# Kernel optimization log

Measured on AMD Instinct MI355X. Metric: run time of the kernel, lower is better.

## Reference

```python
import jax, jax.numpy as jnp
import numpy as np

# Broyden low-rank inverse-Jacobian matvecs. Us: [b,d,e,T], VTs: [b,T,d,e], x: [b,d,e].
# Unwritten history slots are zero, so using the full buffers equals torch's :nstep slicing.

def _matvec(Us, VTs, x):
    VTx = jnp.einsum('btde,bde->bt', VTs, x)
    return -x + jnp.einsum('bdet,bt->bde', Us, VTx)

def _rmatvec(Us, VTs, x):
    xTU = jnp.einsum('bde,bdet->bt', x, Us)
    return -x + jnp.einsum('bt,btde->bde', xTU, VTs)

def broyden(g, x0, threshold, eps):
    """Faithful port of broyden(..., ls=False): line search returns s=1 always."""
    B, D, E = x0.shape
    T = min(threshold, 27)
    gx0 = g(x0)
    init_obj = jnp.linalg.norm(gx0)
    protect = init_obj * (1e6 * E)  # protect_thres = 1e6 * n_elem
    Us0 = jnp.zeros((B, D, E, T), x0.dtype)
    VTs0 = jnp.zeros((B, T, D, E), x0.dtype)

    def cond(s):
        nstep, x, gx, upd, Us, VTs, obj, low, lx, lg = s
        return (obj >= eps) & (nstep < threshold) & (obj <= protect)

    def body(s):
        nstep, x, gx, upd, Us, VTs, obj, low, lx, lg = s
        x_new = x + upd                     # step size s = 1 (ls off)
        gx_new = g(x_new)
        dx, dg = upd, gx_new - gx
        nstep = nstep + 1
        obj_new = jnp.linalg.norm(gx_new)
        better = obj_new < low
        low = jnp.where(better, obj_new, low)
        lx = jnp.where(better, x_new, lx)
        lg = jnp.where(better, gx_new, lg)
        # Broyden rank-1 update of the inverse-Jacobian history
        vT = _rmatvec(Us, VTs, dx)
        denom = jnp.einsum('bde,bde->b', vT, dg)
        u = (dx - _matvec(Us, VTs, dg)) / denom[:, None, None]
        vT = jnp.where(jnp.isnan(vT), 0.0, vT)
        u = jnp.where(jnp.isnan(u), 0.0, u)
        Us = Us.at[:, :, :, (nstep - 1) % T].set(u)
        VTs = VTs.at[:, (nstep - 1) % T].set(vT)
        upd = -_matvec(Us, VTs, gx_new)
        return (nstep, x_new, gx_new, upd, Us, VTs, obj_new, low, lx, lg)

    s0 = (jnp.int32(0), x0, gx0, gx0, Us0, VTs0, init_obj, init_obj, x0, gx0)
    s = jax.lax.while_loop(cond, body, s0)
    return s[8], jnp.linalg.norm(s[9])  # lowest_xest, ||lowest_gx||


def f_layer(z, x, W, U, b):
    return jnp.tanh(z @ W + x @ U + b)


def setup_inputs() -> dict:
    key = jax.random.key(0)
    k1, k2, k3, k4 = jax.random.split(key, 4)
    B, D = 256, 2048
    x = jax.random.normal(k1, (B, D), jnp.float32)
    initial_point = jnp.zeros((B, D), jnp.float32)
    W = jax.random.normal(k2, (D, D), jnp.float32) * (0.4 / np.sqrt(D))  # contractive in z
    U = jax.random.normal(k3, (D, D), jnp.float32) * (1.0 / np.sqrt(D))
    b = jax.random.normal(k4, (D,), jnp.float32) * 0.01
    return {"x": x, "initial_point": initial_point, "W": W, "U": U, "b": b}


def reference(x, initial_point, W, U, b):
    MAX_ITER = 12  # kwargs['max_iter']
    B = x.shape[0]

    def g(z_flat):  # broyd_output_test: f(z, x) - z, flattened to [B, D, 1]
        z = z_flat[..., 0]
        return (f_layer(z, x, W, U, b) - z)[..., None]

    z0 = initial_point.reshape(B, -1, 1)
    out_x, _ = broyden(g, z0, MAX_ITER, 1e-8)
    z = f_layer(out_x[..., 0].reshape(x.shape), x, W, U, b)
    return z
```

## Files before the change

### kernel.cpp

```cpp
#include <hip/hip_runtime.h>
#include <math.h>


#define DD 2048
#define KA 4096
#define KW 2048
#define BB 256
#define BD (BB * DD)
#define TT 12
#define NKS 4

#define ST_S   0
#define ST_A   169
#define ST_B   325
#define ST_PHI 481
#define ST_XI  494
#define ST_XSN 507
#define ST_SZ  1024

typedef unsigned short ushort_t;
typedef _Float16 half_t;
typedef __attribute__((ext_vector_type(8))) short short8;
typedef __attribute__((ext_vector_type(4))) float floatx4;
typedef __attribute__((ext_vector_type(4))) _Float16 half4;

__device__ __forceinline__ ushort_t f2bf(float f) {
    unsigned int u = __float_as_uint(f);
    unsigned int r = (u + 0x7FFFu + ((u >> 16) & 1u)) >> 16;
    return (ushort_t)r;
}
__device__ __forceinline__ float bf2f(ushort_t h) {
    return __uint_as_float(((unsigned int)h) << 16);
}
__device__ __forceinline__ float fast_tanh(float x) {
    float e = __expf(2.f * x);
    return 1.f - 2.f / (e + 1.f);
}
__device__ __forceinline__ void gload_lds16(const void* g, void* l) {
    __builtin_amdgcn_global_load_lds(
        (const __attribute__((address_space(1))) unsigned int*)g,
        (__attribute__((address_space(3))) unsigned int*)l, 16, 0, 0);
}
__device__ __forceinline__ float wave_red(float v) {
#pragma unroll
    for (int off = 32; off > 0; off >>= 1) v += __shfl_down(v, off, 64);
    return v;
}
#define WS() do { asm volatile("s_waitcnt lgkmcnt(0)" ::: "memory"); \
                  __builtin_amdgcn_wave_barrier(); } while (0)

__global__ __launch_bounds__(256)
void prep(const float* __restrict__ W, const float* __restrict__ U,
          ushort_t* __restrict__ Wt, ushort_t* __restrict__ Ut,
          const float* __restrict__ xin, ushort_t* __restrict__ Axx,
          float* __restrict__ stbase) {
    __shared__ ushort_t Hs[64][65];
    const int bid = blockIdx.x;
    const int tid = threadIdx.x;
    if (bid < 2048) {
        const int bz = bid >> 10, by = (bid >> 5) & 31, bx = bid & 31;
        const float* src = bz ? U : W;
        ushort_t* dst = bz ? Ut : Wt;
        const int k0 = by * 64, n0 = bx * 64;
        const int r = tid >> 4, c4 = (tid & 15) * 4;
#pragma unroll
        for (int i = 0; i < 4; ++i) {
            int kr = r + i * 16;
            float4 w = *(const float4*)(src + (size_t)(k0 + kr) * DD + n0 + c4);
            Hs[kr][c4 + 0] = f2bf(w.x); Hs[kr][c4 + 1] = f2bf(w.y);
            Hs[kr][c4 + 2] = f2bf(w.z); Hs[kr][c4 + 3] = f2bf(w.w);
        }
        __syncthreads();
#pragma unroll
        for (int i = 0; i < 4; ++i) {
            int nr = r + i * 16;
            ushort4 hv = { Hs[c4+0][nr], Hs[c4+1][nr], Hs[c4+2][nr], Hs[c4+3][nr] };
            *(ushort4*)(dst + (size_t)(n0 + nr) * KW + (size_t)(k0 + c4)) = hv;
        }
    } else {
        const int i4 = (bid - 2048) * 256 + tid;
        const int idx = i4 * 4;
        const int m = idx >> 11, col = idx & 2047;
        float4 xv = ((const float4*)xin)[i4];
        float a[4] = {xv.x, xv.y, xv.z, xv.w};
        ushort_t hh[4], ll[4];
#pragma unroll
        for (int j = 0; j < 4; ++j) { hh[j] = f2bf(a[j]); ll[j] = f2bf(a[j] - bf2f(hh[j])); }
        ushort4 h = {hh[0],hh[1],hh[2],hh[3]}, l = {ll[0],ll[1],ll[2],ll[3]};
        size_t ab = (size_t)m * KA + col;
        *(ushort4*)(Axx + ab) = h; *(ushort4*)(Axx + ab + DD) = l;
        if (i4 < 65544) {
            float4 z = {0.f, 0.f, 0.f, 0.f};
            ((float4*)stbase)[i4] = z;
        }
    }
}

template<int LDA, int KSLICE, int NIT, int BMOD, typename YT>
__global__ __launch_bounds__(256)
void gemm_t(const ushort_t* __restrict__ A, const ushort_t* __restrict__ Bt,
            YT* __restrict__ y) {
    __shared__ ushort_t As[4][64 * 64];
    __shared__ ushort_t Bs[4][64 * 64];
    const int tid = threadIdx.x;
    const int lane = tid & 63, w = tid >> 6;
    const int bn = blockIdx.x * 64;
    const int mt = blockIdx.y;
    const int ks = blockIdx.z;
    const int waveM = w >> 1, waveN = w & 1;

    const int srow = tid >> 3;
    const int sg = (tid & 7) ^ (srow & 7);
    const ushort_t* Ag = A  + (size_t)(mt * 64 + srow) * LDA + ks * KSLICE + sg * 8;
    const ushort_t* Bg = Bt + (size_t)(bn + srow) * KW + (ks & BMOD) * KSLICE + sg * 8;
    const size_t rsA = (size_t)32 * LDA;
    const size_t rsB = (size_t)32 * KW;

    const int q = lane >> 4, rl = lane & 15;
    int offA[2][2], offB[2][2];
#pragma unroll
    for (int kk = 0; kk < 2; ++kk) {
        int j = kk * 4 + q;
#pragma unroll
        for (int mi = 0; mi < 2; ++mi) {
            int m = waveM * 32 + mi * 16 + rl;
            offA[kk][mi] = (m * 8 + (j ^ (m & 7))) * 8;
        }
#pragma unroll
        for (int ni = 0; ni < 2; ++ni) {
            int n = waveN * 32 + ni * 16 + rl;
            offB[kk][ni] = (n * 8 + (j ^ (n & 7))) * 8;
        }
    }

    floatx4 acc[2][2];
#pragma unroll
    for (int mi = 0; mi < 2; ++mi)
#pragma unroll
        for (int ni = 0; ni < 2; ++ni) acc[mi][ni] = (floatx4){0.f,0.f,0.f,0.f};

#pragma unroll
    for (int t = 0; t < 3; ++t) {
        gload_lds16(Ag,       As[t] + tid * 8);
        gload_lds16(Ag + rsA, As[t] + (256 + tid) * 8);
        gload_lds16(Bg,       Bs[t] + tid * 8);
        gload_lds16(Bg + rsB, Bs[t] + (256 + tid) * 8);
        Ag += 64; Bg += 64;
    }

#pragma unroll
    for (int it = 0; it < NIT; ++it) {
        const int rem = NIT - 1 - it;
        if (rem >= 2)      asm volatile("s_waitcnt vmcnt(8)" ::: "memory");
        else if (rem == 1) asm volatile("s_waitcnt vmcnt(4)" ::: "memory");
        else               asm volatile("s_waitcnt vmcnt(0)" ::: "memory");
        __builtin_amdgcn_s_barrier();
        if (it + 3 < NIT) {
            const int nb4 = (it + 3) & 3;
            gload_lds16(Ag,       As[nb4] + tid * 8);
            gload_lds16(Ag + rsA, As[nb4] + (256 + tid) * 8);
            gload_lds16(Bg,       Bs[nb4] + tid * 8);
            gload_lds16(Bg + rsB, Bs[nb4] + (256 + tid) * 8);
            Ag += 64; Bg += 64;
        }
        const ushort_t* Ab = As[it & 3];
        const ushort_t* Bb = Bs[it & 3];
#pragma unroll
        for (int kk = 0; kk < 2; ++kk) {
            short8 b0 = *(const short8*)(Bb + offB[kk][0]);
            short8 b1 = *(const short8*)(Bb + offB[kk][1]);
#pragma unroll
            for (int mi = 0; mi < 2; ++mi) {
                short8 a = *(const short8*)(Ab + offA[kk][mi]);
                acc[mi][0] = __builtin_amdgcn_mfma_f32_16x16x32_bf16(a, b0, acc[mi][0], 0, 0, 0);
                acc[mi][1] = __builtin_amdgcn_mfma_f32_16x16x32_bf16(a, b1, acc[mi][1], 0, 0, 0);
            }
        }
    }

    YT* yp = y + (size_t)ks * BD;
    const int mb = mt * 64 + waveM * 32 + q * 4;
    const int nb = bn + waveN * 32 + rl;
#pragma unroll
    for (int mi = 0; mi < 2; ++mi)
#pragma unroll
        for (int r = 0; r < 4; ++r) {
            yp[(size_t)(mb + mi * 16 + r) * DD + nb]      = (YT)acc[mi][0][r];
            yp[(size_t)(mb + mi * 16 + r) * DD + nb + 16] = (YT)acc[mi][1][r];
        }
}

__global__ __launch_bounds__(512)
void epi0(const float* __restrict__ y, const float* __restrict__ bias,
          float* __restrict__ c, ushort_t* __restrict__ gxp,
          ushort_t* __restrict__ Azz, float* __restrict__ state,
          float* __restrict__ scal) {
    __shared__ float red[8];
    const int tid = threadIdx.x;
    const int b = blockIdx.x;
    const int col = tid * 4;
    const size_t base = (size_t)b * DD + col;

    float4 cc = *(const float4*)(bias + col);
#pragma unroll
    for (int s = 0; s < NKS; ++s) {
        float4 v = *(const float4*)(y + (size_t)s * BD + base);
        cc.x += v.x; cc.y += v.y; cc.z += v.z; cc.w += v.w;
    }
    *(float4*)(c + base) = cc;
    float4 g = { fast_tanh(cc.x), fast_tanh(cc.y), fast_tanh(cc.z), fast_tanh(cc.w) };
    ushort4 gs = { f2bf(g.x), f2bf(g.y), f2bf(g.z), f2bf(g.w) };
    *(ushort4*)(gxp + base) = gs;
    *(ushort4*)(Azz + base) = gs;

    float pd = g.x*g.x + g.y*g.y + g.z*g.z + g.w*g.w;
    pd = wave_red(pd);
    if ((tid & 63) == 0) red[tid >> 6] = pd;
    __syncthreads();
    if (tid == 0) {
        float t = 0.f;
#pragma unroll
        for (int w2 = 0; w2 < 8; ++w2) t += red[w2];
        float* stb = state + (size_t)b * ST_SZ;
        stb[ST_S + 0]   = t;
        stb[ST_PHI + 0] = 1.f;
        stb[ST_XI + 0]  = 1.f;
        atomicAdd(&scal[0], t);
    }
}

__global__ __launch_bounds__(512)
void broyden_gram(const half_t* __restrict__ yh, const float* __restrict__ c,
                  ushort_t* __restrict__ gxp, ushort_t* __restrict__ Azz,
                  float* __restrict__ state, float* __restrict__ scal, int k)
{
    __shared__ float red[8][16];
    __shared__ float dots[14];
    __shared__ float Sl[169], Al[156], Bl[156], PHl[13], XIl[13];
    __shared__ float newA[14], newB[14], nphi[14];
    __shared__ double dyv[13], dxtu[12], dvdg[12], dcgx[13], dden[1];
    const int tid = threadIdx.x;
    const int lane = tid & 63, w = tid >> 6;
    const int b = blockIdx.x;
    const int p = k - 1;
    float* stb = state + (size_t)b * ST_SZ;

    const int col = tid * 4;
    const size_t base = (size_t)b * DD + col;

    float4 G[12];
#pragma unroll
    for (int j = 0; j < 12; ++j)
        if (j < k) {
            ushort4 gu = *(const ushort4*)(gxp + (size_t)j * BD + base);
            G[j] = (float4){ bf2f(gu.x), bf2f(gu.y), bf2f(gu.z), bf2f(gu.w) };
        }

    float4 pre = *(const float4*)(c + base);
#pragma unroll
    for (int s = 0; s < NKS; ++s) {
        half4 v = *(const half4*)(yh + (size_t)s * BD + base);
        pre.x += (float)v.x; pre.y += (float)v.y;
        pre.z += (float)v.z; pre.w += (float)v.w;
    }

    for (int i = tid; i < 169; i += 512) Sl[i] = stb[ST_S + i];
    for (int i = tid; i < 156; i += 512) { Al[i] = stb[ST_A + i]; Bl[i] = stb[ST_B + i]; }
    if (tid < 13) { PHl[tid] = stb[ST_PHI + tid]; XIl[tid] = stb[ST_XI + tid]; }

    __syncthreads();

    float4 x = {0.f, 0.f, 0.f, 0.f};
#pragma unroll
    for (int j = 0; j < 12; ++j)
        if (j < k) {
            float xc = XIl[j];
            x.x = fmaf(xc, G[j].x, x.x); x.y = fmaf(xc, G[j].y, x.y);
            x.z = fmaf(xc, G[j].z, x.z); x.w = fmaf(xc, G[j].w, x.w);
        }
    float4 gk = { fast_tanh(pre.x) - x.x, fast_tanh(pre.y) - x.y,
                  fast_tanh(pre.z) - x.z, fast_tanh(pre.w) - x.w };

    {
        ushort4 gs = { f2bf(gk.x), f2bf(gk.y), f2bf(gk.z), f2bf(gk.w) };
        *(ushort4*)(gxp + (size_t)k * BD + base) = gs;
    }

#pragma unroll
    for (int j = 0; j < 12; ++j)
        if (j < k) {
            float pd = G[j].x*gk.x + G[j].y*gk.y + G[j].z*gk.z + G[j].w*gk.w;
            pd = wave_red(pd);
            if (lane == 0) red[w][j] = pd;
        }
    {
        float pdk = gk.x*gk.x + gk.y*gk.y + gk.z*gk.z + gk.w*gk.w;
        pdk = wave_red(pdk);
        if (lane == 0) red[w][k] = pdk;
    }
    __syncthreads();

    if (w == 0) {
        if (lane <= k) {
            float s = 0.f;
#pragma unroll
            for (int w2 = 0; w2 < 8; ++w2) s += red[w2][lane];
            dots[lane] = s;
            if (lane == k) atomicAdd(&scal[k], s);
        }
        WS();
        if (lane < k) {
            double s = 0.0;
            for (int j = 0; j < k; ++j) s += (double)Sl[lane*13 + j] * (double)PHl[j];
            dyv[lane] = s;
        }
        WS();
        if (lane < p) {
            double sx = 0.0, sv = 0.0;
            for (int j = 0; j < k; ++j) {
                sx += (double)Al[lane*13 + j] * dyv[j];
                sv += (double)Bl[lane*13 + j] * ((double)dots[j] - (double)Sl[j*13 + (k-1)]);
            }
            dxtu[lane] = sx; dvdg[lane] = sv;
        }
        WS();
        if (lane < k) {
            double s = -(double)PHl[lane];
            for (int t = 0; t < p; ++t) s += dxtu[t] * (double)Bl[t*13 + lane];
            newB[lane] = (float)s;
        }
        WS();
        if (lane == 0) {
            double s = 0.0;
            for (int j = 0; j < k; ++j)
                s += (double)newB[j] * ((double)dots[j] - (double)Sl[j*13 + (k-1)]);
            dden[0] = s;
        }
        if (lane >= 32 && lane < 32 + p) {
            int t = lane - 32;
            double s = 0.0;
            for (int j = 0; j < k; ++j) s += (double)Bl[t*13 + j] * (double)dots[j];
            dcgx[t] = s;
        }
        if (lane == 63) {
            double s = 0.0;
            for (int j = 0; j < k; ++j) s += (double)newB[j] * (double)dots[j];
            dcgx[p] = s;
        }
        WS();
        if (lane <= k) {
            double s = (double)((lane < 13) ? PHl[lane] : 0.f);
            if (lane == k)     s += 1.0;
            if (lane == k - 1) s -= 1.0;
            for (int t = 0; t < p; ++t) s -= dvdg[t] * (double)Al[t*13 + lane];
            newA[lane] = (float)(s / dden[0]);
        }
        WS();
        if (lane <= k) {
            double s = (lane == k) ? 1.0 : 0.0;
            for (int t = 0; t < p; ++t) s -= dcgx[t] * (double)Al[t*13 + lane];
            s -= dcgx[p] * (double)newA[lane];
            nphi[lane] = (float)s;
        }
        WS();
        if (lane <= k) {
            stb[ST_S + k*13 + lane] = dots[lane];
            stb[ST_S + lane*13 + k] = dots[lane];
            stb[ST_A + p*13 + lane] = newA[lane];
            stb[ST_PHI + lane] = nphi[lane];
            float xi_old = (lane < 13) ? XIl[lane] : 0.f;
            stb[ST_XI + lane] = xi_old + nphi[lane];
        }
        if (lane < k) stb[ST_B + p*13 + lane] = newB[lane];
        if (lane < 13) stb[ST_XSN + k*13 + lane] = XIl[lane];
    }
    __syncthreads();

    if (k < TT) {
        float4 xn = x;
#pragma unroll
        for (int j = 0; j < 12; ++j)
            if (j < k) {
                float fc = nphi[j];
                xn.x = fmaf(fc, G[j].x, xn.x); xn.y = fmaf(fc, G[j].y, xn.y);
                xn.z = fmaf(fc, G[j].z, xn.z); xn.w = fmaf(fc, G[j].w, xn.w);
            }
        float fk = nphi[k];
        xn.x = fmaf(fk, gk.x, xn.x); xn.y = fmaf(fk, gk.y, xn.y);
        xn.z = fmaf(fk, gk.z, xn.z); xn.w = fmaf(fk, gk.w, xn.w);

        ushort4 h = { f2bf(xn.x), f2bf(xn.y), f2bf(xn.z), f2bf(xn.w) };
        *(ushort4*)(Azz + base) = h;
    }
}

__global__ __launch_bounds__(256)
void final_out(const ushort_t* __restrict__ gxp, const float* __restrict__ state,
               const float* __restrict__ scal, float* __restrict__ out) {
    const int i4 = blockIdx.x * 256 + threadIdx.x;
    float best = scal[0];
    int bk = 0;
#pragma unroll
    for (int k = 1; k <= TT; ++k) {
        float o = scal[k];
        if (o < best) { best = o; bk = k; }
    }
    const size_t idx = (size_t)i4 * 4;
    const int m = (int)(idx >> 11);
    const float* cf = state + (size_t)m * ST_SZ + ST_XSN + bk * 13;
    ushort4 gb = *(const ushort4*)(gxp + (size_t)bk * BD + idx);
    float4 r = { bf2f(gb.x), bf2f(gb.y), bf2f(gb.z), bf2f(gb.w) };
    for (int j = 0; j < bk; ++j) {
        float c1 = cf[j];
        ushort4 gu = *(const ushort4*)(gxp + (size_t)j * BD + idx);
        r.x = fmaf(c1, bf2f(gu.x), r.x); r.y = fmaf(c1, bf2f(gu.y), r.y);
        r.z = fmaf(c1, bf2f(gu.z), r.z); r.w = fmaf(c1, bf2f(gu.w), r.w);
    }
    ((float4*)out)[i4] = r;
}

extern "C" void kernel_launch(void* const* d_in, const int* in_sizes, int n_in,
                              void* d_out, int out_size, void* d_ws, size_t ws_size,
                              hipStream_t stream) {
    const float* xin  = (const float*)d_in[0];
    const float* W    = (const float*)d_in[2];
    const float* U    = (const float*)d_in[3];
    const float* bias = (const float*)d_in[4];
    float* out = (float*)d_out;

    float* ws = (float*)d_ws;
    float* c      = ws;
    float* y      = ws + 1 * (size_t)BD;
    ushort_t* gxp = (ushort_t*)(ws + 9 * (size_t)BD);
    ushort_t* Axx = (ushort_t*)(ws + 16 * (size_t)BD);
    ushort_t* Azz = (ushort_t*)(ws + 17 * (size_t)BD);
    ushort_t* Wt  = (ushort_t*)(ws + 18 * (size_t)BD);
    ushort_t* Ut  = (ushort_t*)(ws + 22 * (size_t)BD);
    float* state  = ws + 26 * (size_t)BD;
    float* scal   = state + (size_t)BB * ST_SZ;

    prep<<<2560, 256, 0, stream>>>(W, U, Wt, Ut, xin, Axx, state);

    dim3 gg(32, 4, NKS);
    gemm_t<4096, 1024, 16, 1, float><<<gg, 256, 0, stream>>>(Axx, Ut, y);
    epi0<<<BB, 512, 0, stream>>>(y, bias, c, gxp, Azz, state, scal);

    for (int k = 1; k <= TT; ++k) {
        gemm_t<2048, 512, 8, 3, half_t><<<gg, 256, 0, stream>>>(Azz, Wt, (half_t*)y);
        broyden_gram<<<BB, 512, 0, stream>>>((const half_t*)y, c, gxp, Azz, state, scal, k);
    }

    final_out<<<512, 256, 0, stream>>>(gxp, state, scal, out);
}
```

Before: 325.2 us.

## Fuse GEMM and Broyden epilogue into one launch with atomic flag handoff

```diff
diff --git a/kernel.cpp b/kernel.cpp
--- a/kernel.cpp
+++ b/kernel.cpp
@@ -48,6 +48,17 @@
 }
 #define WS() do { asm volatile("s_waitcnt lgkmcnt(0)" ::: "memory"); \
                   __builtin_amdgcn_wave_barrier(); } while (0)
+
+union SharedU {
+    struct { ushort_t As[4][4096]; ushort_t Bs[4][4096]; } g;
+    struct {
+        float red[8][16];
+        float dots[14];
+        float Sl[169], Al[156], Bl[156], PHl[13], XIl[13];
+        float newA[14], newB[14], nphi[14];
+        double dyv[13], dxtu[12], dvdg[12], dcgx[13], dden[1];
+    } b;
+};
 
 __global__ __launch_bounds__(256)
 void prep(const float* __restrict__ W, const float* __restrict__ U,
@@ -89,7 +100,7 @@
         ushort4 h = {hh[0],hh[1],hh[2],hh[3]}, l = {ll[0],ll[1],ll[2],ll[3]};
         size_t ab = (size_t)m * KA + col;
         *(ushort4*)(Axx + ab) = h; *(ushort4*)(Axx + ab + DD) = l;
-        if (i4 < 65544) {
+        if (i4 < 65548) {
             float4 z = {0.f, 0.f, 0.f, 0.f};
             ((float4*)stbase)[i4] = z;
         }
@@ -97,19 +108,21 @@
 }
 
 template<int LDA, int KSLICE, int NIT, int BMOD, typename YT>
-__global__ __launch_bounds__(256)
-void gemm_t(const ushort_t* __restrict__ A, const ushort_t* __restrict__ Bt,
-            YT* __restrict__ y) {
-    __shared__ ushort_t As[4][64 * 64];
-    __shared__ ushort_t Bs[4][64 * 64];
+__device__ __forceinline__ void gemm_part(const ushort_t* __restrict__ A,
+                                          const ushort_t* __restrict__ Bt,
+                                          YT* __restrict__ y, SharedU& sh) {
+    ushort_t (*As)[4096] = sh.g.As;
+    ushort_t (*Bs)[4096] = sh.g.Bs;
     const int tid = threadIdx.x;
+    const bool act = tid < 256;
+    const int bid = blockIdx.x;
+    const int bn = (bid & 31) * 64;
+    const int mt = (bid >> 5) & 3;
+    const int ks = bid >> 7;
     const int lane = tid & 63, w = tid >> 6;
-    const int bn = blockIdx.x * 64;
-    const int mt = blockIdx.y;
-    const int ks = blockIdx.z;
-    const int waveM = w >> 1, waveN = w & 1;
-
-    const int srow = tid >> 3;
+    const int waveM = (w >> 1) & 1, waveN = w & 1;
+
+    const int srow = (tid >> 3) & 31;
     const int sg = (tid & 7) ^ (srow & 7);
     const ushort_t* Ag = A  + (size_t)(mt * 64 + srow) * LDA + ks * KSLICE + sg * 8;
     const ushort_t* Bg = Bt + (size_t)(bn + srow) * KW + (ks & BMOD) * KSLICE + sg * 8;
@@ -139,13 +152,15 @@
 #pragma unroll
         for (int ni = 0; ni < 2; ++ni) acc[mi][ni] = (floatx4){0.f,0.f,0.f,0.f};
 
-#pragma unroll
-    for (int t = 0; t < 3; ++t) {
-        gload_lds16(Ag,       As[t] + tid * 8);
-        gload_lds16(Ag + rsA, As[t] + (256 + tid) * 8);
-        gload_lds16(Bg,       Bs[t] + tid * 8);
-        gload_lds16(Bg + rsB, Bs[t] + (256 + tid) * 8);
-        Ag += 64; Bg += 64;
+    if (act) {
+#pragma unroll
+        for (int t = 0; t < 3; ++t) {
+            gload_lds16(Ag,       As[t] + tid * 8);
+            gload_lds16(Ag + rsA, As[t] + (256 + tid) * 8);
+            gload_lds16(Bg,       Bs[t] + tid * 8);
+            gload_lds16(Bg + rsB, Bs[t] + (256 + tid) * 8);
+            Ag += 64; Bg += 64;
+        }
     }
 
 #pragma unroll
@@ -156,97 +171,122 @@
         else               asm volatile("s_waitcnt vmcnt(0)" ::: "memory");
         __builtin_amdgcn_s_barrier();
         if (it + 3 < NIT) {
-            const int nb4 = (it + 3) & 3;
-            gload_lds16(Ag,       As[nb4] + tid * 8);
-            gload_lds16(Ag + rsA, As[nb4] + (256 + tid) * 8);
-            gload_lds16(Bg,       Bs[nb4] + tid * 8);
-            gload_lds16(Bg + rsB, Bs[nb4] + (256 + tid) * 8);
-            Ag += 64; Bg += 64;
-        }
-        const ushort_t* Ab = As[it & 3];
-        const ushort_t* Bb = Bs[it & 3];
-#pragma unroll
-        for (int kk = 0; kk < 2; ++kk) {
-            short8 b0 = *(const short8*)(Bb + offB[kk][0]);
-            short8 b1 = *(const short8*)(Bb + offB[kk][1]);
-#pragma unroll
-            for (int mi = 0; mi < 2; ++mi) {
-                short8 a = *(const short8*)(Ab + offA[kk][mi]);
-                acc[mi][0] = __builtin_amdgcn_mfma_f32_16x16x32_bf16(a, b0, acc[mi][0], 0, 0, 0);
-                acc[mi][1] = __builtin_amdgcn_mfma_f32_16x16x32_bf16(a, b1, acc[mi][1], 0, 0, 0);
+            if (act) {
+                const int nb4 = (it + 3) & 3;
+                gload_lds16(Ag,       As[nb4] + tid * 8);
+                gload_lds16(Ag + rsA, As[nb4] + (256 + tid) * 8);
+                gload_lds16(Bg,       Bs[nb4] + tid * 8);
+                gload_lds16(Bg + rsB, Bs[nb4] + (256 + tid) * 8);
+                Ag += 64; Bg += 64;
             }
         }
-    }
-
-    YT* yp = y + (size_t)ks * BD;
-    const int mb = mt * 64 + waveM * 32 + q * 4;
-    const int nb = bn + waveN * 32 + rl;
-#pragma unroll
-    for (int mi = 0; mi < 2; ++mi)
-#pragma unroll
-        for (int r = 0; r < 4; ++r) {
-            yp[(size_t)(mb + mi * 16 + r) * DD + nb]      = (YT)acc[mi][0][r];
-            yp[(size_t)(mb + mi * 16 + r) * DD + nb + 16] = (YT)acc[mi][1][r];
-        }
-}
-
+        if (act) {
+            const ushort_t* Ab = As[it & 3];
+            const ushort_t* Bb = Bs[it & 3];
+#pragma unroll
+            for (int kk = 0; kk < 2; ++kk) {
+                short8 b0 = *(const short8*)(Bb + offB[kk][0]);
+                short8 b1 = *(const short8*)(Bb + offB[kk][1]);
+#pragma unroll
+                for (int mi = 0; mi < 2; ++mi) {
+                    short8 a = *(const short8*)(Ab + offA[kk][mi]);
+                    acc[mi][0] = __builtin_amdgcn_mfma_f32_16x16x32_bf16(a, b0, acc[mi][0], 0, 0, 0);
+                    acc[mi][1] = __builtin_amdgcn_mfma_f32_16x16x32_bf16(a, b1, acc[mi][1], 0, 0, 0);
+                }
+            }
+        }
+    }
+
+    if (act) {
+        YT* yp = y + (size_t)ks * BD;
+        const int mb = mt * 64 + waveM * 32 + q * 4;
+        const int nb = bn + waveN * 32 + rl;
+#pragma unroll
+        for (int mi = 0; mi < 2; ++mi)
+#pragma unroll
+            for (int r = 0; r < 4; ++r) {
+                yp[(size_t)(mb + mi * 16 + r) * DD + nb]      = (YT)acc[mi][0][r];
+                yp[(size_t)(mb + mi * 16 + r) * DD + nb + 16] = (YT)acc[mi][1][r];
+            }
+    }
+}
+
+__device__ __forceinline__ void wait_flag(unsigned int* flagp) {
+    __syncthreads();
+    if (threadIdx.x == 0) {
+        while (__hip_atomic_load(flagp, __ATOMIC_RELAXED, __HIP_MEMORY_SCOPE_AGENT) < 512u)
+            __builtin_amdgcn_s_sleep(2);
+        __threadfence();
+    }
+    __syncthreads();
+}
+__device__ __forceinline__ void signal_flag(unsigned int* flagp) {
+    __syncthreads();
+    if (threadIdx.x == 0) {
+        __threadfence();
+        __hip_atomic_fetch_add(flagp, 1u, __ATOMIC_RELEASE, __HIP_MEMORY_SCOPE_AGENT);
+    }
+}
+
+template<int LDA, int KSLICE, int NIT, int BMOD, typename YT, bool K0>
 __global__ __launch_bounds__(512)
-void epi0(const float* __restrict__ y, const float* __restrict__ bias,
-          float* __restrict__ c, ushort_t* __restrict__ gxp,
-          ushort_t* __restrict__ Azz, float* __restrict__ state,
-          float* __restrict__ scal) {
-    __shared__ float red[8];
+void fused(const ushort_t* __restrict__ A, const ushort_t* __restrict__ Bt,
+           YT* __restrict__ y, const float* __restrict__ bias,
+           float* __restrict__ c, ushort_t* __restrict__ gxp,
+           ushort_t* __restrict__ Azz, float* __restrict__ state,
+           float* __restrict__ scal, unsigned int* __restrict__ flagp, int k)
+{
+    __shared__ SharedU sh;
+    const int bid = blockIdx.x;
     const int tid = threadIdx.x;
-    const int b = blockIdx.x;
+
+    if (bid < 512) {
+        gemm_part<LDA, KSLICE, NIT, BMOD, YT>(A, Bt, y, sh);
+        signal_flag(flagp);
+        return;
+    }
+
+    const int b = bid - 512;
+    const int lane = tid & 63, w = tid >> 6;
     const int col = tid * 4;
     const size_t base = (size_t)b * DD + col;
-
-    float4 cc = *(const float4*)(bias + col);
-#pragma unroll
-    for (int s = 0; s < NKS; ++s) {
-        float4 v = *(const float4*)(y + (size_t)s * BD + base);
-        cc.x += v.x; cc.y += v.y; cc.z += v.z; cc.w += v.w;
-    }
-    *(float4*)(c + base) = cc;
-    float4 g = { fast_tanh(cc.x), fast_tanh(cc.y), fast_tanh(cc.z), fast_tanh(cc.w) };
-    ushort4 gs = { f2bf(g.x), f2bf(g.y), f2bf(g.z), f2bf(g.w) };
-    *(ushort4*)(gxp + base) = gs;
-    *(ushort4*)(Azz + base) = gs;
-
-    float pd = g.x*g.x + g.y*g.y + g.z*g.z + g.w*g.w;
-    pd = wave_red(pd);
-    if ((tid & 63) == 0) red[tid >> 6] = pd;
-    __syncthreads();
-    if (tid == 0) {
-        float t = 0.f;
-#pragma unroll
-        for (int w2 = 0; w2 < 8; ++w2) t += red[w2];
-        float* stb = state + (size_t)b * ST_SZ;
-        stb[ST_S + 0]   = t;
-        stb[ST_PHI + 0] = 1.f;
-        stb[ST_XI + 0]  = 1.f;
-        atomicAdd(&scal[0], t);
-    }
-}
-
-__global__ __launch_bounds__(512)
-void broyden_gram(const half_t* __restrict__ yh, const float* __restrict__ c,
-                  ushort_t* __restrict__ gxp, ushort_t* __restrict__ Azz,
-                  float* __restrict__ state, float* __restrict__ scal, int k)
-{
-    __shared__ float red[8][16];
-    __shared__ float dots[14];
-    __shared__ float Sl[169], Al[156], Bl[156], PHl[13], XIl[13];
-    __shared__ float newA[14], newB[14], nphi[14];
-    __shared__ double dyv[13], dxtu[12], dvdg[12], dcgx[13], dden[1];
-    const int tid = threadIdx.x;
-    const int lane = tid & 63, w = tid >> 6;
-    const int b = blockIdx.x;
+    float* stb = state + (size_t)b * ST_SZ;
+
+    if (K0) {
+        float4 cc = *(const float4*)(bias + col);
+        wait_flag(flagp);
+#pragma unroll
+        for (int s = 0; s < NKS; ++s) {
+            float4 v = *(const float4*)((const float*)y + (size_t)s * BD + base);
+            cc.x += v.x; cc.y += v.y; cc.z += v.z; cc.w += v.w;
+        }
+        *(float4*)(c + base) = cc;
+        float4 g = { fast_tanh(cc.x), fast_tanh(cc.y), fast_tanh(cc.z), fast_tanh(cc.w) };
+        ushort4 gs = { f2bf(g.x), f2bf(g.y), f2bf(g.z), f2bf(g.w) };
+        *(ushort4*)(gxp + base) = gs;
+        *(ushort4*)(Azz + base) = gs;
+
+        float pd = g.x*g.x + g.y*g.y + g.z*g.z + g.w*g.w;
+        pd = wave_red(pd);
+        if (lane == 0) sh.b.red[w][0] = pd;
+        __syncthreads();
+        if (tid == 0) {
+            float t = 0.f;
+#pragma unroll
+            for (int w2 = 0; w2 < 8; ++w2) t += sh.b.red[w2][0];
+            stb[ST_S + 0]   = t;
+            stb[ST_PHI + 0] = 1.f;
+            stb[ST_XI + 0]  = 1.f;
+            atomicAdd(&scal[0], t);
+        }
+        return;
+    }
+
     const int p = k - 1;
-    float* stb = state + (size_t)b * ST_SZ;
-
-    const int col = tid * 4;
-    const size_t base = (size_t)b * DD + col;
+
+    for (int i = tid; i < 169; i += 512) sh.b.Sl[i] = stb[ST_S + i];
+    for (int i = tid; i < 156; i += 512) { sh.b.Al[i] = stb[ST_A + i]; sh.b.Bl[i] = stb[ST_B + i]; }
+    if (tid < 13) { sh.b.PHl[tid] = stb[ST_PHI + tid]; sh.b.XIl[tid] = stb[ST_XI + tid]; }
 
     float4 G[12];
 #pragma unroll
@@ -255,8 +295,11 @@
             ushort4 gu = *(const ushort4*)(gxp + (size_t)j * BD + base);
             G[j] = (float4){ bf2f(gu.x), bf2f(gu.y), bf2f(gu.z), bf2f(gu.w) };
         }
-
     float4 pre = *(const float4*)(c + base);
+
+    wait_flag(flagp);
+
+    const half_t* yh = (const half_t*)y;
 #pragma unroll
     for (int s = 0; s < NKS; ++s) {
         half4 v = *(const half4*)(yh + (size_t)s * BD + base);
@@ -264,17 +307,11 @@
         pre.z += (float)v.z; pre.w += (float)v.w;
     }
 
-    for (int i = tid; i < 169; i += 512) Sl[i] = stb[ST_S + i];
-    for (int i = tid; i < 156; i += 512) { Al[i] = stb[ST_A + i]; Bl[i] = stb[ST_B + i]; }
-    if (tid < 13) { PHl[tid] = stb[ST_PHI + tid]; XIl[tid] = stb[ST_XI + tid]; }
-
-    __syncthreads();
-
     float4 x = {0.f, 0.f, 0.f, 0.f};
 #pragma unroll
     for (int j = 0; j < 12; ++j)
         if (j < k) {
-            float xc = XIl[j];
+            float xc = sh.b.XIl[j];
             x.x = fmaf(xc, G[j].x, x.x); x.y = fmaf(xc, G[j].y, x.y);
             x.z = fmaf(xc, G[j].z, x.z); x.w = fmaf(xc, G[j].w, x.w);
         }
@@ -291,12 +328,12 @@
         if (j < k) {
             float pd = G[j].x*gk.x + G[j].y*gk.y + G[j].z*gk.z + G[j].w*gk.w;
             pd = wave_red(pd);
-            if (lane == 0) red[w][j] = pd;
+            if (lane == 0) sh.b.red[w][j] = pd;
         }
     {
         float pdk = gk.x*gk.x + gk.y*gk.y + gk.z*gk.z + gk.w*gk.w;
         pdk = wave_red(pdk);
-        if (lane == 0) red[w][k] = pdk;
+        if (lane == 0) sh.b.red[w][k] = pdk;
     }
     __syncthreads();
 
@@ -304,75 +341,75 @@
         if (lane <= k) {
             float s = 0.f;
 #pragma unroll
-            for (int w2 = 0; w2 < 8; ++w2) s += red[w2][lane];
-            dots[lane] = s;
+            for (int w2 = 0; w2 < 8; ++w2) s += sh.b.red[w2][lane];
+            sh.b.dots[lane] = s;
             if (lane == k) atomicAdd(&scal[k], s);
         }
         WS();
         if (lane < k) {
             double s = 0.0;
-            for (int j = 0; j < k; ++j) s += (double)Sl[lane*13 + j] * (double)PHl[j];
-            dyv[lane] = s;
+            for (int j = 0; j < k; ++j) s += (double)sh.b.Sl[lane*13 + j] * (double)sh.b.PHl[j];
+            sh.b.dyv[lane] = s;
         }
         WS();
         if (lane < p) {
             double sx = 0.0, sv = 0.0;
             for (int j = 0; j < k; ++j) {
-                sx += (double)Al[lane*13 + j] * dyv[j];
-                sv += (double)Bl[lane*13 + j] * ((double)dots[j] - (double)Sl[j*13 + (k-1)]);
+                sx += (double)sh.b.Al[lane*13 + j] * sh.b.dyv[j];
+                sv += (double)sh.b.Bl[lane*13 + j] * ((double)sh.b.dots[j] - (double)sh.b.Sl[j*13 + (k-1)]);
             }
-            dxtu[lane] = sx; dvdg[lane] = sv;
+            sh.b.dxtu[lane] = sx; sh.b.dvdg[lane] = sv;
         }
         WS();
         if (lane < k) {
-            double s = -(double)PHl[lane];
-            for (int t = 0; t < p; ++t) s += dxtu[t] * (double)Bl[t*13 + lane];
-            newB[lane] = (float)s;
+            double s = -(double)sh.b.PHl[lane];
+            for (int t = 0; t < p; ++t) s += sh.b.dxtu[t] * (double)sh.b.Bl[t*13 + lane];
+            sh.b.newB[lane] = (float)s;
         }
         WS();
         if (lane == 0) {
             double s = 0.0;
             for (int j = 0; j < k; ++j)
-                s += (double)newB[j] * ((double)dots[j] - (double)Sl[j*13 + (k-1)]);
-            dden[0] = s;
+                s += (double)sh.b.newB[j] * ((double)sh.b.dots[j] - (double)sh.b.Sl[j*13 + (k-1)]);
+            sh.b.dden[0] = s;
         }
         if (lane >= 32 && lane < 32 + p) {
             int t = lane - 32;
             double s = 0.0;
-            for (int j = 0; j < k; ++j) s += (double)Bl[t*13 + j] * (double)dots[j];
-            dcgx[t] = s;
+            for (int j = 0; j < k; ++j) s += (double)sh.b.Bl[t*13 + j] * (double)sh.b.dots[j];
+            sh.b.dcgx[t] = s;
         }
         if (lane == 63) {
             double s = 0.0;
-            for (int j = 0; j < k; ++j) s += (double)newB[j] * (double)dots[j];
-            dcgx[p] = s;
+            for (int j = 0; j < k; ++j) s += (double)sh.b.newB[j] * (double)sh.b.dots[j];
+            sh.b.dcgx[p] = s;
         }
         WS();
         if (lane <= k) {
-            double s = (double)((lane < 13) ? PHl[lane] : 0.f);
+            double s = (double)((lane < 13) ? sh.b.PHl[lane] : 0.f);
             if (lane == k)     s += 1.0;
             if (lane == k - 1) s -= 1.0;
-            for (int t = 0; t < p; ++t) s -= dvdg[t] * (double)Al[t*13 + lane];
-            newA[lane] = (float)(s / dden[0]);
+            for (int t = 0; t < p; ++t) s -= sh.b.dvdg[t] * (double)sh.b.Al[t*13 + lane];
+            sh.b.newA[lane] = (float)(s / sh.b.dden[0]);
         }
         WS();
         if (lane <= k) {
             double s = (lane == k) ? 1.0 : 0.0;
-            for (int t = 0; t < p; ++t) s -= dcgx[t] * (double)Al[t*13 + lane];
-            s -= dcgx[p] * (double)newA[lane];
-            nphi[lane] = (float)s;
+            for (int t = 0; t < p; ++t) s -= sh.b.dcgx[t] * (double)sh.b.Al[t*13 + lane];
+            s -= sh.b.dcgx[p] * (double)sh.b.newA[lane];
+            sh.b.nphi[lane] = (float)s;
         }
         WS();
         if (lane <= k) {
-            stb[ST_S + k*13 + lane] = dots[lane];
-            stb[ST_S + lane*13 + k] = dots[lane];
-            stb[ST_A + p*13 + lane] = newA[lane];
-            stb[ST_PHI + lane] = nphi[lane];
-            float xi_old = (lane < 13) ? XIl[lane] : 0.f;
-            stb[ST_XI + lane] = xi_old + nphi[lane];
-        }
-        if (lane < k) stb[ST_B + p*13 + lane] = newB[lane];
-        if (lane < 13) stb[ST_XSN + k*13 + lane] = XIl[lane];
+            stb[ST_S + k*13 + lane] = sh.b.dots[lane];
+            stb[ST_S + lane*13 + k] = sh.b.dots[lane];
+            stb[ST_A + p*13 + lane] = sh.b.newA[lane];
+            stb[ST_PHI + lane] = sh.b.nphi[lane];
+            float xi_old = (lane < 13) ? sh.b.XIl[lane] : 0.f;
+            stb[ST_XI + lane] = xi_old + sh.b.nphi[lane];
+        }
+        if (lane < k) stb[ST_B + p*13 + lane] = sh.b.newB[lane];
+        if (lane < 13) stb[ST_XSN + k*13 + lane] = sh.b.XIl[lane];
     }
     __syncthreads();
 
@@ -381,11 +418,11 @@
 #pragma unroll
         for (int j = 0; j < 12; ++j)
             if (j < k) {
-                float fc = nphi[j];
+                float fc = sh.b.nphi[j];
                 xn.x = fmaf(fc, G[j].x, xn.x); xn.y = fmaf(fc, G[j].y, xn.y);
                 xn.z = fmaf(fc, G[j].z, xn.z); xn.w = fmaf(fc, G[j].w, xn.w);
             }
-        float fk = nphi[k];
+        float fk = sh.b.nphi[k];
         xn.x = fmaf(fk, gk.x, xn.x); xn.y = fmaf(fk, gk.y, xn.y);
         xn.z = fmaf(fk, gk.z, xn.z); xn.w = fmaf(fk, gk.w, xn.w);
 
@@ -438,16 +475,16 @@
     ushort_t* Ut  = (ushort_t*)(ws + 22 * (size_t)BD);
     float* state  = ws + 26 * (size_t)BD;
     float* scal   = state + (size_t)BB * ST_SZ;
+    unsigned int* flags = (unsigned int*)(scal + 32);
 
     prep<<<2560, 256, 0, stream>>>(W, U, Wt, Ut, xin, Axx, state);
 
-    dim3 gg(32, 4, NKS);
-    gemm_t<4096, 1024, 16, 1, float><<<gg, 256, 0, stream>>>(Axx, Ut, y);
-    epi0<<<BB, 512, 0, stream>>>(y, bias, c, gxp, Azz, state, scal);
+    fused<4096, 1024, 16, 1, float, true><<<768, 512, 0, stream>>>(
+        Axx, Ut, y, bias, c, gxp, Azz, state, scal, flags + 0, 0);
 
     for (int k = 1; k <= TT; ++k) {
-        gemm_t<2048, 512, 8, 3, half_t><<<gg, 256, 0, stream>>>(Azz, Wt, (half_t*)y);
-        broyden_gram<<<BB, 512, 0, stream>>>((const half_t*)y, c, gxp, Azz, state, scal, k);
+        fused<2048, 512, 8, 3, half_t, false><<<768, 512, 0, stream>>>(
+            Azz, Wt, (half_t*)y, bias, c, gxp, Azz, state, scal, flags + k, k);
     }
 
     final_out<<<512, 256, 0, stream>>>(gxp, state, scal, out);
```

New measurement: 831.4 us. 2.56x slower.
